# Kernel optimization log

Hardware: AMD Instinct MI355X
Metric: run time of the kernel (lower is better)

## Reference

```python
import jax, jax.numpy as jnp
from jax import lax
import numpy as np

T, B, I, H = 2048, 64, 256, 256


def setup_inputs() -> dict:
    key = jax.random.key(0)
    ks = jax.random.split(key, 7)
    s = 1.0 / np.sqrt(H)  # torch default init scale, keeps gates unsaturated
    return {
        "x": jax.random.normal(ks[0], (T, B, I), dtype=jnp.float32),
        "h0": jax.random.normal(ks[1], (1, B, H), dtype=jnp.float32),
        "c0": jax.random.normal(ks[2], (1, B, H), dtype=jnp.float32),
        "w_ih": jax.random.normal(ks[3], (4 * H, I), dtype=jnp.float32) * s,
        "w_hh": jax.random.normal(ks[4], (4 * H, H), dtype=jnp.float32) * s,
        "b_ih": jax.random.normal(ks[5], (4 * H,), dtype=jnp.float32) * s,
        "b_hh": jax.random.normal(ks[6], (4 * H,), dtype=jnp.float32) * s,
    }


def _lstm_scan(x, h0, c0, w_ih, w_hh, b_ih, b_hh):
    # Precompute input projections for all timesteps in one GEMM: [T,B,4H]
    xg = jnp.einsum("tbi,gi->tbg", x, w_ih) + (b_ih + b_hh)
    w_hh_t = w_hh.T  # [H,4H]

    def step(carry, xg_t):
        h, c = carry  # [B,H] each
        g = xg_t + h @ w_hh_t  # [B,4H], PyTorch gate order i,f,g,o
        i_g, f_g, g_g, o_g = jnp.split(g, 4, axis=-1)
        i_g = jax.nn.sigmoid(i_g)
        f_g = jax.nn.sigmoid(f_g)
        g_g = jnp.tanh(g_g)
        o_g = jax.nn.sigmoid(o_g)
        c_new = f_g * c + i_g * g_g
        h_new = o_g * jnp.tanh(c_new)
        return (h_new, c_new), (h_new, c_new)

    (_, _), (hy, cy) = lax.scan(step, (h0[0], c0[0]), xg)
    # match torch.stack of per-step (num_directions=1, B, H) states -> [T,1,B,H]
    return hy[:, None, :, :], cy[:, None, :, :]


def reference(x, h0, c0, w_ih, w_hh, b_ih, b_hh):
    hy, cy = _lstm_scan(x, h0, c0, w_ih, w_hh, b_ih, b_hh)
    return hy, cy, (hy[-1], cy[-1])
```

## Files before the change

### kernel.cpp

```cpp
#include <hip/hip_runtime.h>

typedef short s16x8 __attribute__((ext_vector_type(8)));
typedef short s16x4 __attribute__((ext_vector_type(4)));
typedef float f32x4 __attribute__((ext_vector_type(4)));
typedef unsigned long long u64;

#define T_N 2048
#define B_N 64
#define H_N 256
#define I_N 256
#define HY_BYTES ((size_t)134217728)
#define WS_V2 131072
#define EXCH_BYTES 65536
#define WS_V1 (EXCH_BYTES + 256)

static __device__ __forceinline__ short f2bf(float f) {
    unsigned u = __builtin_bit_cast(unsigned, f);
    u += 0x7FFFu + ((u >> 16) & 1u);
    return (short)(u >> 16);
}
static __device__ __forceinline__ float bf2f(short h) {
    unsigned u = ((unsigned)(unsigned short)h) << 16;
    return __builtin_bit_cast(float, u);
}
static __device__ __forceinline__ float e2c(float a) {
    return __builtin_amdgcn_exp2f(fminf(a, 126.0f));
}
static __device__ __forceinline__ s16x4 ntl4(const void* p) {
    return __builtin_nontemporal_load((const s16x4*)p);
}

#define C1 1.44269504088896340f
#define C2 2.88539008177792681f

#define MFMA(a, b, c) __builtin_amdgcn_mfma_f32_16x16x32_bf16(a, b, c, 0, 0, 0)

__global__ void zero_flags(char* __restrict__ ws) {
    if (threadIdx.x < 64) ((unsigned*)(ws + EXCH_BYTES))[threadIdx.x] = 0u;
}

__global__ __launch_bounds__(512) void xg_gemm(
        const float* __restrict__ x, const float* __restrict__ w_ih,
        const float* __restrict__ b_ih, const float* __restrict__ b_hh,
        char* __restrict__ out)
{
    const int tid  = threadIdx.x;
    const int wave = tid >> 6;
    const int lane = tid & 63;
    const int l15  = lane & 15;
    const int kg   = lane >> 4;

    __shared__ short Blds[8192];

    const int m16 = blockIdx.x * 8 + wave;
    const int by  = blockIdx.y;
    const int n0  = by * 256;

    const float* xrow = x + (size_t)(m16 * 16 + l15) * I_N;

    f32x4 acc[16] = {};

#pragma unroll 1
    for (int ks = 0; ks < 8; ++ks) {
        __syncthreads();
#pragma unroll
        for (int h = 0; h < 2; ++h) {
            int nl = (tid >> 2) + h * 128;
            int c  = tid & 3;
            const float* wp = w_ih + (size_t)(n0 + nl) * I_N + ks * 32 + c * 8;
            f32x4 w0 = *(const f32x4*)(wp);
            f32x4 w1 = *(const f32x4*)(wp + 4);
            s16x8 bv;
            bv[0]=f2bf(w0[0]); bv[1]=f2bf(w0[1]); bv[2]=f2bf(w0[2]); bv[3]=f2bf(w0[3]);
            bv[4]=f2bf(w1[0]); bv[5]=f2bf(w1[1]); bv[6]=f2bf(w1[2]); bv[7]=f2bf(w1[3]);
            int dt = nl >> 4;
            int lp = (nl & 15) + 16 * c;
            *(s16x8*)(&Blds[(dt * 64 + lp) * 8]) = bv;
        }
        __syncthreads();
        const float* ap = xrow + ks * 32 + kg * 8;
        f32x4 a0 = *(const f32x4*)(ap);
        f32x4 a1 = *(const f32x4*)(ap + 4);
        s16x8 av;
        av[0]=f2bf(a0[0]); av[1]=f2bf(a0[1]); av[2]=f2bf(a0[2]); av[3]=f2bf(a0[3]);
        av[4]=f2bf(a1[0]); av[5]=f2bf(a1[1]); av[6]=f2bf(a1[2]); av[7]=f2bf(a1[3]);
#pragma unroll
        for (int dt = 0; dt < 16; ++dt) {
            s16x8 bv = *(const s16x8*)(&Blds[(dt * 64 + lane) * 8]);
            acc[dt] = MFMA(av, bv, acc[dt]);
        }
    }

    const int t = m16 >> 2;
    const int g = m16 & 3;
#pragma unroll
    for (int dt = 0; dt < 16; ++dt) {
        int tau = by * 16 + dt;
        int n   = tau * 16 + l15;
        float bias = b_ih[n] + b_hh[n];
        float scale = ((tau >> 4) == 2) ? -C2 : -C1;
        size_t base = (tau < 32)
            ? ((size_t)t * 65536 + (size_t)g * 16384 + (size_t)tau * 512)
            : (HY_BYTES + (size_t)t * 65536 + (size_t)g * 16384 + (size_t)(tau - 32) * 512);
        s16x4 o;
        o[0] = f2bf(scale * (acc[dt][0] + bias));
        o[1] = f2bf(scale * (acc[dt][1] + bias));
        o[2] = f2bf(scale * (acc[dt][2] + bias));
        o[3] = f2bf(scale * (acc[dt][3] + bias));
        *(s16x4*)(out + base + lane * 8) = o;
    }
}

__global__ __launch_bounds__(512)
__attribute__((amdgpu_waves_per_eu(2, 2)))
void lstm_rec8v4(
        const float* __restrict__ h0, const float* __restrict__ c0,
        const float* __restrict__ w_hh, char* __restrict__ out,
        char* __restrict__ ws)
{
    const int b    = blockIdx.x;
    const int g    = b & 3;
    const int hf   = b >> 2;
    const int tid  = threadIdx.x;
    const int w    = tid >> 6;
    const int lane = tid & 63;
    const int l15  = lane & 15;
    const int kg   = lane >> 4;

    const int tc   = hf * 8 + w;
    const int ptc  = (hf ^ 1) * 8 + w;
    const int col  = tc * 16 + l15;
    const int pcol = ptc * 16 + l15;

    __shared__ short hlds[2][4096];

    u64* exch = (u64*)ws;
    const size_t myx = (size_t)b * 1024 + (size_t)w * 128 + (size_t)lane * 2;
    const size_t pbx = (size_t)(b ^ 4) * 1024 + (size_t)w * 128 + (size_t)lane * 2;

    s16x8 wreg[4][8];
#pragma unroll
    for (int q = 0; q < 4; ++q) {
        const int tau = 16 * q + tc;
        const float scale = (q == 2) ? -C2 : -C1;
        const float* wp = w_hh + (size_t)(tau * 16 + l15) * H_N;
#pragma unroll
        for (int ks = 0; ks < 8; ++ks) {
            const float* p = wp + ks * 32 + kg * 8;
            f32x4 w0 = *(const f32x4*)(p);
            f32x4 w1 = *(const f32x4*)(p + 4);
            s16x8 v;
            v[0]=f2bf(scale*w0[0]); v[1]=f2bf(scale*w0[1]);
            v[2]=f2bf(scale*w0[2]); v[3]=f2bf(scale*w0[3]);
            v[4]=f2bf(scale*w1[0]); v[5]=f2bf(scale*w1[1]);
            v[6]=f2bf(scale*w1[2]); v[7]=f2bf(scale*w1[3]);
            wreg[q][ks] = v;
        }
    }

    {
        const int row  = tid >> 5;
        const int col0 = (tid & 31) * 8;
        const float* hp = h0 + (size_t)(g * 16 + row) * H_N + col0;
        const int sw = (row & 7) << 4;
#pragma unroll
        for (int j = 0; j < 8; ++j) {
            int byte = row * 512 + ((2 * (col0 + j)) ^ sw);
            *(short*)((char*)hlds[0] + byte) = f2bf(hp[j]);
        }
    }

    float cst[4];
#pragma unroll
    for (int r = 0; r < 4; ++r)
        cst[r] = c0[(size_t)(g * 16 + kg * 4 + r) * H_N + col];

    float hnew[4] = {};
    unsigned dead = 0;

    __syncthreads();

    const char* p_xg0 = out + (size_t)g * 16384 + (size_t)tc * 512 + (size_t)lane * 8;
    const char* p_xg1 = p_xg0 + 16 * 512;
    const char* p_xg2 = out + HY_BYTES + (size_t)g * 16384 + (size_t)tc * 512 + (size_t)lane * 8;
    const char* p_xg3 = p_xg2 + 16 * 512;
    char* st_h = out + (size_t)(g * 16 + kg * 4) * 1024 + (size_t)col * 4;
    char* st_c = st_h + HY_BYTES;

    const int amask = (l15 & 7) << 4;

    s16x4 xg[4];

#define XG_LOAD(T) do {                                                       \
        const size_t _o = ((size_t)(T) << 16);                                \
        xg[0] = ntl4(p_xg0 + _o);  xg[1] = ntl4(p_xg1 + _o);                  \
        xg[2] = ntl4(p_xg2 + _o);  xg[3] = ntl4(p_xg3 + _o);                  \
    } while (0)

    XG_LOAD(0);
    asm volatile("s_waitcnt vmcnt(0)" ::: "memory");

#define STEP(PAR, T) do {                                                     \
                     \
        f32x4 acc[4];                                                         \
        _Pragma("unroll")                                                     \
        for (int q = 0; q < 4; ++q) {                                         \
            acc[q][0] = bf2f(xg[q][0]); acc[q][1] = bf2f(xg[q][1]);           \
            acc[q][2] = bf2f(xg[q][2]); acc[q][3] = bf2f(xg[q][3]);           \
        }                                                                     \
             \
        _Pragma("unroll")                                                     \
        for (int ks = 0; ks < 8; ++ks) {                                      \
            s16x8 av = *(const s16x8*)((const char*)hlds[PAR] +               \
                            l15 * 512 + ((ks * 64 + kg * 16) ^ amask));       \
            acc[0] = MFMA(av, wreg[0][ks], acc[0]);                           \
            acc[1] = MFMA(av, wreg[1][ks], acc[1]);                           \
            acc[2] = MFMA(av, wreg[2][ks], acc[2]);                           \
            acc[3] = MFMA(av, wreg[3][ks], acc[3]);                           \
        }                                                                     \
                  \
        unsigned pk0, pk1;                                                    \
        {                                                                     \
            _Pragma("unroll")                                                 \
            for (int r = 0; r < 4; ++r) {                                     \
                float Ei = e2c(acc[0][r]);                                    \
                float Ef = e2c(acc[1][r]);                                    \
                float Eg = e2c(acc[2][r]);                                    \
                float Eo = e2c(acc[3][r]);                                    \
                float ai = 1.0f + Ei, af = 1.0f + Ef;                         \
                float ag = 1.0f + Eg, ao = 1.0f + Eo;                         \
                float r1 = __builtin_amdgcn_rcpf(ai * af);                    \
                float gi = r1 * af;                                           \
                float gf = r1 * ai;                                           \
                float r2 = __builtin_amdgcn_rcpf(ag * ao);                    \
                float go = r2 * ag;                                           \
                float tg = 2.0f * (r2 * ao) - 1.0f;                           \
                float c  = gf * cst[r] + gi * tg;                             \
                cst[r] = c;                                                   \
                float Ec = e2c(-C2 * c);                                      \
                float tc_ = 2.0f * __builtin_amdgcn_rcpf(1.0f + Ec) - 1.0f;   \
                hnew[r] = go * tc_;                                           \
            }                                                                 \
            unsigned s0 = (unsigned short)f2bf(hnew[0]);                      \
            unsigned s1 = (unsigned short)f2bf(hnew[1]);                      \
            unsigned s2 = (unsigned short)f2bf(hnew[2]);                      \
            unsigned s3 = (unsigned short)f2bf(hnew[3]);                      \
            pk0 = s0 | (s1 << 16);                                            \
            pk1 = s2 | (s3 << 16);                                            \
        }                                                                     \
        u64 v0 = 0, v1 = 0;                                                   \
        if ((T) + 1 < T_N) {                                                  \
                             \
            u64 c64 = ((u64)(unsigned)((T) + 1)) << 32;                       \
            u64* _m = exch + (size_t)(PAR) * 8192 + myx;                      \
            __hip_atomic_store(_m,     (u64)pk0 | c64,                        \
                               __ATOMIC_RELAXED, __HIP_MEMORY_SCOPE_AGENT);   \
            __hip_atomic_store(_m + 1, (u64)pk1 | c64,                        \
                               __ATOMIC_RELAXED, __HIP_MEMORY_SCOPE_AGENT);   \
                     \
            const u64* _p = exch + (size_t)(PAR) * 8192 + pbx;                \
            v0 = __hip_atomic_load(_p,     __ATOMIC_RELAXED,                  \
                                   __HIP_MEMORY_SCOPE_AGENT);                 \
            v1 = __hip_atomic_load(_p + 1, __ATOMIC_RELAXED,                  \
                                   __HIP_MEMORY_SCOPE_AGENT);                 \
        }                                                                     \
          \
        {                                                                     \
            char* _hp = st_h + ((size_t)(T) << 16);                           \
            char* _cp = st_c + ((size_t)(T) << 16);                           \
            _Pragma("unroll")                                                 \
            for (int r = 0; r < 4; ++r) {                                     \
                *(float*)(_hp + r * 1024) = hnew[r];                          \
                *(float*)(_cp + r * 1024) = cst[r];                           \
            }                                                                 \
        }                                                                     \
                                            \
        _Pragma("unroll")                                                     \
        for (int r = 0; r < 4; ++r) {                                         \
            int row = kg * 4 + r;                                             \
            int byte = row * 512 + ((2 * col) ^ ((row & 7) << 4));            \
            unsigned v = (r < 2) ? pk0 : pk1;                                 \
            *(short*)((char*)hlds[(PAR) ^ 1] + byte) =                        \
                (short)((r & 1) ? (v >> 16) : v);                             \
        }                                                                     \
        if ((T) + 1 < T_N) {                                                  \
                            \
            XG_LOAD((T) + 1);                                                 \
                             \
            const unsigned tgt = (unsigned)((T) + 1);                         \
            int ok = ((unsigned)(v0 >> 32) == tgt) &                          \
                     ((unsigned)(v1 >> 32) == tgt);                           \
            if (!__all(ok) && !dead) {                                        \
                const u64* _p = exch + (size_t)(PAR) * 8192 + pbx;            \
                unsigned spins = 0;                                           \
                for (;;) {                                                    \
                    v0 = __hip_atomic_load(_p,     __ATOMIC_RELAXED,          \
                                           __HIP_MEMORY_SCOPE_AGENT);         \
                    v1 = __hip_atomic_load(_p + 1, __ATOMIC_RELAXED,          \
                                           __HIP_MEMORY_SCOPE_AGENT);         \
                    ok = ((unsigned)(v0 >> 32) == tgt) &                      \
                         ((unsigned)(v1 >> 32) == tgt);                       \
                    if (__all(ok)) break;                                     \
                    __builtin_amdgcn_s_sleep(1);                              \
                    if (++spins > 16384u) { dead = 1; break; }                \
                }                                                             \
            }                                                                 \
                          \
            _Pragma("unroll")                                                 \
            for (int r = 0; r < 4; ++r) {                                     \
                int row = kg * 4 + r;                                         \
                int byte = row * 512 + ((2 * pcol) ^ ((row & 7) << 4));       \
                unsigned v = (r < 2) ? (unsigned)v0 : (unsigned)v1;           \
                *(short*)((char*)hlds[(PAR) ^ 1] + byte) =                    \
                    (short)((r & 1) ? (v >> 16) : v);                         \
            }                                                                 \
        }                                                                     \
                     \
        asm volatile("s_waitcnt lgkmcnt(0)" ::: "memory");                    \
        __builtin_amdgcn_s_barrier();                                         \
        asm volatile("" ::: "memory");                                        \
    } while (0)

#pragma unroll 1
    for (int tt = 0; tt < T_N; tt += 2) {
        STEP(0, tt);
        STEP(1, tt + 1);
    }

    {
        char* fh = out + 2 * HY_BYTES + (size_t)(g * 16 + kg * 4) * 1024 + (size_t)col * 4;
        char* fc = fh + 65536;
#pragma unroll
        for (int r = 0; r < 4; ++r) {
            *(float*)(fh + r * 1024) = hnew[r];
            *(float*)(fc + r * 1024) = cst[r];
        }
    }
#undef STEP
#undef XG_LOAD
}

__global__ __launch_bounds__(512)
__attribute__((amdgpu_waves_per_eu(2, 2)))
void lstm_rec8(
        const float* __restrict__ h0, const float* __restrict__ c0,
        const float* __restrict__ w_hh, char* __restrict__ out,
        char* __restrict__ ws)
{
    const int b    = blockIdx.x;
    const int g    = b & 3;
    const int hf   = b >> 2;
    const int tid  = threadIdx.x;
    const int w    = tid >> 6;
    const int lane = tid & 63;
    const int l15  = lane & 15;
    const int kg   = lane >> 4;

    const int tc   = hf * 8 + w;
    const int ptc  = (hf ^ 1) * 8 + w;
    const int col  = tc * 16 + l15;
    const int pcol = ptc * 16 + l15;

    __shared__ short hlds[2][4096];

    u64* exch = (u64*)ws;
    unsigned* flags = (unsigned*)(ws + EXCH_BYTES);
    const size_t myx = ((size_t)b * 8 + w) * 64 + lane;
    const size_t pbx = ((size_t)(b ^ 4) * 8 + w) * 64 + lane;
    unsigned* myflag = &flags[b * 8 + w];
    unsigned* pflag  = &flags[(b ^ 4) * 8 + w];

    s16x8 wreg[4][8];
#pragma unroll
    for (int q = 0; q < 4; ++q) {
        const int tau = 16 * q + tc;
        const float scale = (q == 2) ? -C2 : -C1;
        const float* wp = w_hh + (size_t)(tau * 16 + l15) * H_N;
#pragma unroll
        for (int ks = 0; ks < 8; ++ks) {
            const float* p = wp + ks * 32 + kg * 8;
            f32x4 w0 = *(const f32x4*)(p);
            f32x4 w1 = *(const f32x4*)(p + 4);
            s16x8 v;
            v[0]=f2bf(scale*w0[0]); v[1]=f2bf(scale*w0[1]);
            v[2]=f2bf(scale*w0[2]); v[3]=f2bf(scale*w0[3]);
            v[4]=f2bf(scale*w1[0]); v[5]=f2bf(scale*w1[1]);
            v[6]=f2bf(scale*w1[2]); v[7]=f2bf(scale*w1[3]);
            wreg[q][ks] = v;
        }
    }

    {
        const int row  = tid >> 5;
        const int col0 = (tid & 31) * 8;
        const float* hp = h0 + (size_t)(g * 16 + row) * H_N + col0;
        const int sw = (row & 7) << 4;
#pragma unroll
        for (int j = 0; j < 8; ++j) {
            int byte = row * 512 + ((2 * (col0 + j)) ^ sw);
            *(short*)((char*)hlds[0] + byte) = f2bf(hp[j]);
        }
    }

    float cst[4];
#pragma unroll
    for (int r = 0; r < 4; ++r)
        cst[r] = c0[(size_t)(g * 16 + kg * 4 + r) * H_N + col];

    float hnew[4] = {};
    unsigned dead = 0;

    __syncthreads();

    const char* p_xg0 = out + (size_t)g * 16384 + (size_t)tc * 512 + (size_t)lane * 8;
    const char* p_xg1 = p_xg0 + 16 * 512;
    const char* p_xg2 = out + HY_BYTES + (size_t)g * 16384 + (size_t)tc * 512 + (size_t)lane * 8;
    const char* p_xg3 = p_xg2 + 16 * 512;
    char* st_h = out + (size_t)(g * 16 + kg * 4) * 1024 + (size_t)col * 4;
    char* st_c = st_h + HY_BYTES;

    const int amask = (l15 & 7) << 4;

    s16x4 xg[4];

#define XG_LOAD(T) do {                                                       \
        const size_t _o = ((size_t)(T) << 16);                                \
        xg[0] = ntl4(p_xg0 + _o);  xg[1] = ntl4(p_xg1 + _o);                  \
        xg[2] = ntl4(p_xg2 + _o);  xg[3] = ntl4(p_xg3 + _o);                  \
    } while (0)

    XG_LOAD(0);
    asm volatile("s_waitcnt vmcnt(0)" ::: "memory");

#define STEP(PAR, T) do {                                                     \
        if ((T) > 0) {                                                        \
            char* _hp = st_h + ((size_t)((T) - 1) << 16);                     \
            char* _cp = st_c + ((size_t)((T) - 1) << 16);                     \
            _Pragma("unroll")                                                 \
            for (int r = 0; r < 4; ++r) {                                     \
                *(float*)(_hp + r * 1024) = hnew[r];                          \
                *(float*)(_cp + r * 1024) = cst[r];                           \
            }                                                                 \
        }                                                                     \
        unsigned fv = __hip_atomic_load(pflag, __ATOMIC_RELAXED,              \
                                        __HIP_MEMORY_SCOPE_AGENT);            \
        f32x4 acc[4];                                                         \
        _Pragma("unroll")                                                     \
        for (int q = 0; q < 4; ++q) {                                         \
            acc[q][0] = bf2f(xg[q][0]); acc[q][1] = bf2f(xg[q][1]);           \
            acc[q][2] = bf2f(xg[q][2]); acc[q][3] = bf2f(xg[q][3]);           \
        }                                                                     \
        _Pragma("unroll")                                                     \
        for (int ks = 0; ks < 8; ++ks) {                                      \
            s16x8 av = *(const s16x8*)((const char*)hlds[PAR] +               \
                            l15 * 512 + ((ks * 64 + kg * 16) ^ amask));       \
            acc[0] = MFMA(av, wreg[0][ks], acc[0]);                           \
            acc[1] = MFMA(av, wreg[1][ks], acc[1]);                           \
            acc[2] = MFMA(av, wreg[2][ks], acc[2]);                           \
            acc[3] = MFMA(av, wreg[3][ks], acc[3]);                           \
        }                                                                     \
        unsigned pk0, pk1;                                                    \
        {                                                                     \
            _Pragma("unroll")                                                 \
            for (int r = 0; r < 4; ++r) {                                     \
                float Ei = e2c(acc[0][r]);                                    \
                float Ef = e2c(acc[1][r]);                                    \
                float Eg = e2c(acc[2][r]);                                    \
                float Eo = e2c(acc[3][r]);                                    \
                float ai = 1.0f + Ei, af = 1.0f + Ef;                         \
                float ag = 1.0f + Eg, ao = 1.0f + Eo;                         \
                float r1 = __builtin_amdgcn_rcpf(ai * af);                    \
                float gi = r1 * af;                                           \
                float gf = r1 * ai;                                           \
                float r2 = __builtin_amdgcn_rcpf(ag * ao);                    \
                float go = r2 * ag;                                           \
                float tg = 2.0f * (r2 * ao) - 1.0f;                           \
                float c  = gf * cst[r] + gi * tg;                             \
                cst[r] = c;                                                   \
                float Ec = e2c(-C2 * c);                                      \
                float tc_ = 2.0f * __builtin_amdgcn_rcpf(1.0f + Ec) - 1.0f;   \
                hnew[r] = go * tc_;                                           \
            }                                                                 \
            unsigned s0 = (unsigned short)f2bf(hnew[0]);                      \
            unsigned s1 = (unsigned short)f2bf(hnew[1]);                      \
            unsigned s2 = (unsigned short)f2bf(hnew[2]);                      \
            unsigned s3 = (unsigned short)f2bf(hnew[3]);                      \
            pk0 = s0 | (s1 << 16);                                            \
            pk1 = s2 | (s3 << 16);                                            \
            _Pragma("unroll")                                                 \
            for (int r = 0; r < 4; ++r) {                                     \
                int row = kg * 4 + r;                                         \
                int byte = row * 512 + ((2 * col) ^ ((row & 7) << 4));        \
                unsigned v = (r < 2) ? pk0 : pk1;                             \
                *(short*)((char*)hlds[(PAR) ^ 1] + byte) =                    \
                    (short)((r & 1) ? (v >> 16) : v);                         \
            }                                                                 \
        }                                                                     \
        if ((T) + 1 < T_N) {                                                  \
            unsigned long long val = ((unsigned long long)pk1 << 32) | pk0;   \
            __hip_atomic_store(exch + (size_t)(PAR) * 4096 + myx, val,        \
                               __ATOMIC_RELAXED, __HIP_MEMORY_SCOPE_AGENT);   \
            asm volatile("s_waitcnt vmcnt(0)" ::: "memory");                  \
            if (lane == 0)                                                    \
                __hip_atomic_store(myflag, (unsigned)((T) + 1),               \
                                   __ATOMIC_RELAXED,                          \
                                   __HIP_MEMORY_SCOPE_AGENT);                 \
            XG_LOAD((T) + 1);                                                 \
            if (fv < (unsigned)((T) + 1) && !dead) {                          \
                unsigned spins = 0;                                           \
                while (__hip_atomic_load(pflag, __ATOMIC_RELAXED,             \
                                         __HIP_MEMORY_SCOPE_AGENT)           \
                       < (unsigned)((T) + 1)) {                               \
                    __builtin_amdgcn_s_sleep(1);                              \
                    if (++spins > 16384u) { dead = 1; break; }                \
                }                                                             \
            }                                                                 \
            unsigned long long pvv = __hip_atomic_load(                       \
                exch + (size_t)(PAR) * 4096 + pbx,                            \
                __ATOMIC_RELAXED, __HIP_MEMORY_SCOPE_AGENT);                  \
            _Pragma("unroll")                                                 \
            for (int r = 0; r < 4; ++r) {                                     \
                int row = kg * 4 + r;                                         \
                int byte = row * 512 + ((2 * pcol) ^ ((row & 7) << 4));       \
                *(short*)((char*)hlds[(PAR) ^ 1] + byte) =                    \
                    (short)(pvv >> (16 * r));                                 \
            }                                                                 \
        }                                                                     \
        asm volatile("s_waitcnt lgkmcnt(0)" ::: "memory");                    \
        __builtin_amdgcn_s_barrier();                                         \
        asm volatile("" ::: "memory");                                        \
    } while (0)

#pragma unroll 1
    for (int tt = 0; tt < T_N; tt += 2) {
        STEP(0, tt);
        STEP(1, tt + 1);
    }

    {
        char* hp = st_h + ((size_t)(T_N - 1) << 16);
        char* cp = st_c + ((size_t)(T_N - 1) << 16);
        char* fh = out + 2 * HY_BYTES + (size_t)(g * 16 + kg * 4) * 1024 + (size_t)col * 4;
        char* fc = fh + 65536;
#pragma unroll
        for (int r = 0; r < 4; ++r) {
            *(float*)(hp + r * 1024) = hnew[r];
            *(float*)(cp + r * 1024) = cst[r];
            *(float*)(fh + r * 1024) = hnew[r];
            *(float*)(fc + r * 1024) = cst[r];
        }
    }
#undef STEP
#undef XG_LOAD
}

extern "C" void kernel_launch(void* const* d_in, const int* in_sizes, int n_in,
                              void* d_out, int out_size, void* d_ws, size_t ws_size,
                              hipStream_t stream) {
    (void)in_sizes; (void)n_in; (void)out_size;
    const float* x    = (const float*)d_in[0];
    const float* h0   = (const float*)d_in[1];
    const float* c0   = (const float*)d_in[2];
    const float* w_ih = (const float*)d_in[3];
    const float* w_hh = (const float*)d_in[4];
    const float* b_ih = (const float*)d_in[5];
    const float* b_hh = (const float*)d_in[6];
    char* out = (char*)d_out;

    if (ws_size >= WS_V2) {
        xg_gemm<<<dim3(1024, 4), 512, 0, stream>>>(x, w_ih, b_ih, b_hh, out);
        lstm_rec8v4<<<8, 512, 0, stream>>>(h0, c0, w_hh, out, (char*)d_ws);
    } else {
        zero_flags<<<1, 64, 0, stream>>>((char*)d_ws);
        xg_gemm<<<dim3(1024, 4), 512, 0, stream>>>(x, w_ih, b_ih, b_hh, out);
        lstm_rec8<<<8, 512, 0, stream>>>(h0, c0, w_hh, out, (char*)d_ws);
    }
}
```

Before: 5.141 ms.

## Split recurrent matmul to overlap local-half MFMAs with peer h exchange wait

Result: slower. 18.33 ms (+256.6%).

```diff
diff --git a/kernel.cpp b/kernel.cpp
--- a/kernel.cpp
+++ b/kernel.cpp
@@ -113,7 +113,7 @@
 
 __global__ __launch_bounds__(512)
 __attribute__((amdgpu_waves_per_eu(2, 2)))
-void lstm_rec8v4(
+void lstm_rec8v5(
         const float* __restrict__ h0, const float* __restrict__ c0,
         const float* __restrict__ w_hh, char* __restrict__ out,
         char* __restrict__ ws)
@@ -131,6 +131,8 @@
     const int ptc  = (hf ^ 1) * 8 + w;
     const int col  = tc * 16 + l15;
     const int pcol = ptc * 16 + l15;
+    const int oks  = 4 * hf;
+    const int pks  = 4 * (hf ^ 1);
 
     __shared__ short hlds[2][4096];
 
@@ -197,74 +199,53 @@
         xg[2] = ntl4(p_xg2 + _o);  xg[3] = ntl4(p_xg3 + _o);                  \
     } while (0)
 
-    XG_LOAD(0);
-    asm volatile("s_waitcnt vmcnt(0)" ::: "memory");
-
-#define STEP(PAR, T) do {                                                     \
-                     \
-        f32x4 acc[4];                                                         \
-        _Pragma("unroll")                                                     \
-        for (int q = 0; q < 4; ++q) {                                         \
-            acc[q][0] = bf2f(xg[q][0]); acc[q][1] = bf2f(xg[q][1]);           \
-            acc[q][2] = bf2f(xg[q][2]); acc[q][3] = bf2f(xg[q][3]);           \
-        }                                                                     \
-             \
-        _Pragma("unroll")                                                     \
-        for (int ks = 0; ks < 8; ++ks) {                                      \
-            s16x8 av = *(const s16x8*)((const char*)hlds[PAR] +               \
-                            l15 * 512 + ((ks * 64 + kg * 16) ^ amask));       \
-            acc[0] = MFMA(av, wreg[0][ks], acc[0]);                           \
-            acc[1] = MFMA(av, wreg[1][ks], acc[1]);                           \
-            acc[2] = MFMA(av, wreg[2][ks], acc[2]);                           \
-            acc[3] = MFMA(av, wreg[3][ks], acc[3]);                           \
-        }                                                                     \
-                  \
-        unsigned pk0, pk1;                                                    \
-        {                                                                     \
-            _Pragma("unroll")                                                 \
-            for (int r = 0; r < 4; ++r) {                                     \
-                float Ei = e2c(acc[0][r]);                                    \
-                float Ef = e2c(acc[1][r]);                                    \
-                float Eg = e2c(acc[2][r]);                                    \
-                float Eo = e2c(acc[3][r]);                                    \
-                float ai = 1.0f + Ei, af = 1.0f + Ef;                         \
-                float ag = 1.0f + Eg, ao = 1.0f + Eo;                         \
-                float r1 = __builtin_amdgcn_rcpf(ai * af);                    \
-                float gi = r1 * af;                                           \
-                float gf = r1 * ai;                                           \
-                float r2 = __builtin_amdgcn_rcpf(ag * ao);                    \
-                float go = r2 * ag;                                           \
-                float tg = 2.0f * (r2 * ao) - 1.0f;                           \
-                float c  = gf * cst[r] + gi * tg;                             \
-                cst[r] = c;                                                   \
-                float Ec = e2c(-C2 * c);                                      \
-                float tc_ = 2.0f * __builtin_amdgcn_rcpf(1.0f + Ec) - 1.0f;   \
-                hnew[r] = go * tc_;                                           \
-            }                                                                 \
-            unsigned s0 = (unsigned short)f2bf(hnew[0]);                      \
-            unsigned s1 = (unsigned short)f2bf(hnew[1]);                      \
-            unsigned s2 = (unsigned short)f2bf(hnew[2]);                      \
-            unsigned s3 = (unsigned short)f2bf(hnew[3]);                      \
-            pk0 = s0 | (s1 << 16);                                            \
-            pk1 = s2 | (s3 << 16);                                            \
-        }                                                                     \
-        u64 v0 = 0, v1 = 0;                                                   \
+#define ACT_PACK(pk0, pk1) do {                                               \
+        _Pragma("unroll")                                                     \
+        for (int r = 0; r < 4; ++r) {                                         \
+            float Ei = e2c(acc[0][r]);                                        \
+            float Ef = e2c(acc[1][r]);                                        \
+            float Eg = e2c(acc[2][r]);                                        \
+            float Eo = e2c(acc[3][r]);                                        \
+            float ai = 1.0f + Ei, af = 1.0f + Ef;                             \
+            float ag = 1.0f + Eg, ao = 1.0f + Eo;                             \
+            float r1 = __builtin_amdgcn_rcpf(ai * af);                        \
+            float gi = r1 * af;                                               \
+            float gf = r1 * ai;                                               \
+            float r2 = __builtin_amdgcn_rcpf(ag * ao);                        \
+            float go = r2 * ag;                                               \
+            float tg = 2.0f * (r2 * ao) - 1.0f;                               \
+            float c  = gf * cst[r] + gi * tg;                                 \
+            cst[r] = c;                                                       \
+            float Ec = e2c(-C2 * c);                                          \
+            float tc_ = 2.0f * __builtin_amdgcn_rcpf(1.0f + Ec) - 1.0f;       \
+            hnew[r] = go * tc_;                                               \
+        }                                                                     \
+        unsigned s0 = (unsigned short)f2bf(hnew[0]);                          \
+        unsigned s1 = (unsigned short)f2bf(hnew[1]);                          \
+        unsigned s2 = (unsigned short)f2bf(hnew[2]);                          \
+        unsigned s3 = (unsigned short)f2bf(hnew[3]);                          \
+        pk0 = s0 | (s1 << 16);                                                \
+        pk1 = s2 | (s3 << 16);                                                \
+    } while (0)
+
+#define TAIL(PAR, T, pk0, pk1) do {                                           \
         if ((T) + 1 < T_N) {                                                  \
-                             \
             u64 c64 = ((u64)(unsigned)((T) + 1)) << 32;                       \
             u64* _m = exch + (size_t)(PAR) * 8192 + myx;                      \
             __hip_atomic_store(_m,     (u64)pk0 | c64,                        \
                                __ATOMIC_RELAXED, __HIP_MEMORY_SCOPE_AGENT);   \
             __hip_atomic_store(_m + 1, (u64)pk1 | c64,                        \
                                __ATOMIC_RELAXED, __HIP_MEMORY_SCOPE_AGENT);   \
-                     \
-            const u64* _p = exch + (size_t)(PAR) * 8192 + pbx;                \
-            v0 = __hip_atomic_load(_p,     __ATOMIC_RELAXED,                  \
-                                   __HIP_MEMORY_SCOPE_AGENT);                 \
-            v1 = __hip_atomic_load(_p + 1, __ATOMIC_RELAXED,                  \
-                                   __HIP_MEMORY_SCOPE_AGENT);                 \
-        }                                                                     \
-          \
+        }                                                                     \
+        _Pragma("unroll")                                                     \
+        for (int r = 0; r < 4; ++r) {                                         \
+            int row = kg * 4 + r;                                             \
+            int byte = row * 512 + ((2 * col) ^ ((row & 7) << 4));            \
+            unsigned v = (r < 2) ? pk0 : pk1;                                 \
+            *(short*)((char*)hlds[(PAR) ^ 1] + byte) =                        \
+                (short)((r & 1) ? (v >> 16) : v);                             \
+        }                                                                     \
+        if ((T) + 1 < T_N) XG_LOAD((T) + 1);                                  \
         {                                                                     \
             char* _hp = st_h + ((size_t)(T) << 16);                           \
             char* _cp = st_c + ((size_t)(T) << 16);                           \
@@ -274,58 +255,106 @@
                 *(float*)(_cp + r * 1024) = cst[r];                           \
             }                                                                 \
         }                                                                     \
-                                            \
-        _Pragma("unroll")                                                     \
-        for (int r = 0; r < 4; ++r) {                                         \
-            int row = kg * 4 + r;                                             \
-            int byte = row * 512 + ((2 * col) ^ ((row & 7) << 4));            \
-            unsigned v = (r < 2) ? pk0 : pk1;                                 \
-            *(short*)((char*)hlds[(PAR) ^ 1] + byte) =                        \
-                (short)((r & 1) ? (v >> 16) : v);                             \
-        }                                                                     \
-        if ((T) + 1 < T_N) {                                                  \
-                            \
-            XG_LOAD((T) + 1);                                                 \
-                             \
-            const unsigned tgt = (unsigned)((T) + 1);                         \
-            int ok = ((unsigned)(v0 >> 32) == tgt) &                          \
-                     ((unsigned)(v1 >> 32) == tgt);                           \
-            if (!__all(ok) && !dead) {                                        \
-                const u64* _p = exch + (size_t)(PAR) * 8192 + pbx;            \
-                unsigned spins = 0;                                           \
-                for (;;) {                                                    \
-                    v0 = __hip_atomic_load(_p,     __ATOMIC_RELAXED,          \
-                                           __HIP_MEMORY_SCOPE_AGENT);         \
-                    v1 = __hip_atomic_load(_p + 1, __ATOMIC_RELAXED,          \
-                                           __HIP_MEMORY_SCOPE_AGENT);         \
-                    ok = ((unsigned)(v0 >> 32) == tgt) &                      \
-                         ((unsigned)(v1 >> 32) == tgt);                       \
-                    if (__all(ok)) break;                                     \
-                    __builtin_amdgcn_s_sleep(1);                              \
-                    if (++spins > 16384u) { dead = 1; break; }                \
-                }                                                             \
-            }                                                                 \
-                          \
-            _Pragma("unroll")                                                 \
-            for (int r = 0; r < 4; ++r) {                                     \
-                int row = kg * 4 + r;                                         \
-                int byte = row * 512 + ((2 * pcol) ^ ((row & 7) << 4));       \
-                unsigned v = (r < 2) ? (unsigned)v0 : (unsigned)v1;           \
-                *(short*)((char*)hlds[(PAR) ^ 1] + byte) =                    \
-                    (short)((r & 1) ? (v >> 16) : v);                         \
-            }                                                                 \
-        }                                                                     \
-                     \
         asm volatile("s_waitcnt lgkmcnt(0)" ::: "memory");                    \
         __builtin_amdgcn_s_barrier();                                         \
         asm volatile("" ::: "memory");                                        \
     } while (0)
 
+    XG_LOAD(0);
+    asm volatile("s_waitcnt vmcnt(0)" ::: "memory");
+
+    {
+        f32x4 acc[4];
+#pragma unroll
+        for (int q = 0; q < 4; ++q) {
+            acc[q][0] = bf2f(xg[q][0]); acc[q][1] = bf2f(xg[q][1]);
+            acc[q][2] = bf2f(xg[q][2]); acc[q][3] = bf2f(xg[q][3]);
+        }
+#pragma unroll
+        for (int ks = 0; ks < 8; ++ks) {
+            s16x8 av = *(const s16x8*)((const char*)hlds[0] +
+                            l15 * 512 + ((ks * 64 + kg * 16) ^ amask));
+            acc[0] = MFMA(av, wreg[0][ks], acc[0]);
+            acc[1] = MFMA(av, wreg[1][ks], acc[1]);
+            acc[2] = MFMA(av, wreg[2][ks], acc[2]);
+            acc[3] = MFMA(av, wreg[3][ks], acc[3]);
+        }
+        unsigned pk0, pk1;
+        ACT_PACK(pk0, pk1);
+        TAIL(0, 0, pk0, pk1);
+    }
+
+#define STEP(PAR, T) do {                                                     \
+                         \
+        f32x4 acc[4];                                                         \
+        _Pragma("unroll")                                                     \
+        for (int q = 0; q < 4; ++q) {                                         \
+            acc[q][0] = bf2f(xg[q][0]); acc[q][1] = bf2f(xg[q][1]);           \
+            acc[q][2] = bf2f(xg[q][2]); acc[q][3] = bf2f(xg[q][3]);           \
+        }                                                                     \
+        _Pragma("unroll")                                                     \
+        for (int s = 0; s < 4; ++s) {                                         \
+            const int ks = oks + s;                                           \
+            s16x8 av = *(const s16x8*)((const char*)hlds[PAR] +               \
+                            l15 * 512 + ((ks * 64 + kg * 16) ^ amask));       \
+            acc[0] = MFMA(av, wreg[0][ks], acc[0]);                           \
+            acc[1] = MFMA(av, wreg[1][ks], acc[1]);                           \
+            acc[2] = MFMA(av, wreg[2][ks], acc[2]);                           \
+            acc[3] = MFMA(av, wreg[3][ks], acc[3]);                           \
+        }                                                                     \
+                         \
+        u64 v0 = 0, v1 = 0;                                                   \
+        if (!dead) {                                                          \
+            const u64* _p = exch + (size_t)((PAR) ^ 1) * 8192 + pbx;          \
+            const unsigned tgt = (unsigned)(T);                               \
+            unsigned spins = 0;                                               \
+            for (;;) {                                                        \
+                v0 = __hip_atomic_load(_p,     __ATOMIC_RELAXED,              \
+                                       __HIP_MEMORY_SCOPE_AGENT);             \
+                v1 = __hip_atomic_load(_p + 1, __ATOMIC_RELAXED,              \
+                                       __HIP_MEMORY_SCOPE_AGENT);             \
+                int ok = ((unsigned)(v0 >> 32) == tgt) &                      \
+                         ((unsigned)(v1 >> 32) == tgt);                       \
+                if (__all(ok)) break;                                         \
+                __builtin_amdgcn_s_sleep(1);                                  \
+                if (++spins > 16384u) { dead = 1; break; }                    \
+            }                                                                 \
+        }                                                                     \
+               \
+        _Pragma("unroll")                                                     \
+        for (int r = 0; r < 4; ++r) {                                         \
+            int row = kg * 4 + r;                                             \
+            int byte = row * 512 + ((2 * pcol) ^ ((row & 7) << 4));           \
+            unsigned v = (r < 2) ? (unsigned)v0 : (unsigned)v1;               \
+            *(short*)((char*)hlds[PAR] + byte) =                              \
+                (short)((r & 1) ? (v >> 16) : v);                             \
+        }                                                                     \
+        asm volatile("s_waitcnt lgkmcnt(0)" ::: "memory");                    \
+        __builtin_amdgcn_s_barrier();                                         \
+        asm volatile("" ::: "memory");                                        \
+                                \
+        _Pragma("unroll")                                                     \
+        for (int s = 0; s < 4; ++s) {                                         \
+            const int ks = pks + s;                                           \
+            s16x8 av = *(const s16x8*)((const char*)hlds[PAR] +               \
+                            l15 * 512 + ((ks * 64 + kg * 16) ^ amask));       \
+            acc[0] = MFMA(av, wreg[0][ks], acc[0]);                           \
+            acc[1] = MFMA(av, wreg[1][ks], acc[1]);                           \
+            acc[2] = MFMA(av, wreg[2][ks], acc[2]);                           \
+            acc[3] = MFMA(av, wreg[3][ks], acc[3]);                           \
+        }                                                                     \
+            \
+        unsigned pk0, pk1;                                                    \
+        ACT_PACK(pk0, pk1);                                                   \
+        TAIL(PAR, T, pk0, pk1);                                               \
+    } while (0)
+
 #pragma unroll 1
-    for (int tt = 0; tt < T_N; tt += 2) {
-        STEP(0, tt);
-        STEP(1, tt + 1);
-    }
+    for (int t = 1; t + 1 < T_N; t += 2) {
+        STEP(1, t);
+        STEP(0, t + 1);
+    }
+    STEP(1, T_N - 1);
 
     {
         char* fh = out + 2 * HY_BYTES + (size_t)(g * 16 + kg * 4) * 1024 + (size_t)col * 4;
@@ -337,6 +366,8 @@
         }
     }
 #undef STEP
+#undef TAIL
+#undef ACT_PACK
 #undef XG_LOAD
 }
 
@@ -569,7 +600,7 @@
 
     if (ws_size >= WS_V2) {
         xg_gemm<<<dim3(1024, 4), 512, 0, stream>>>(x, w_ih, b_ih, b_hh, out);
-        lstm_rec8v4<<<8, 512, 0, stream>>>(h0, c0, w_hh, out, (char*)d_ws);
+        lstm_rec8v5<<<8, 512, 0, stream>>>(h0, c0, w_hh, out, (char*)d_ws);
     } else {
         zero_flags<<<1, 64, 0, stream>>>((char*)d_ws);
         xg_gemm<<<dim3(1024, 4), 512, 0, stream>>>(x, w_ih, b_ih, b_hh, out);
```
